# Performance work log

Hardware: AMD Instinct MI355X
Metric: run time of the kernel (lower is better)

Reference implementation:

```python
import jax, jax.numpy as jnp
import numpy as np

B, T, C, HEAD = 4, 4096, 1024, 64
SCALE = 1.0 / (C ** 0.5)  # module divides by embedding_size**0.5, not head_size**0.5


def setup_inputs() -> dict:
    key = jax.random.key(0)
    kx, kq, kk, kv = jax.random.split(key, 4)
    x = jax.random.normal(kx, (B, T, C), dtype=jnp.float32)
    # nn.Linear(C, head_size, bias=False) weights, stored as (C, head_size) for x @ W
    Wq = jax.random.normal(kq, (C, HEAD), dtype=jnp.float32) * (1.0 / np.sqrt(C))
    Wk = jax.random.normal(kk, (C, HEAD), dtype=jnp.float32) * (1.0 / np.sqrt(C))
    Wv = jax.random.normal(kv, (C, HEAD), dtype=jnp.float32) * (1.0 / np.sqrt(C))
    return {"x": x, "Wq": Wq, "Wk": Wk, "Wv": Wv}


def reference(x, Wq, Wk, Wv):
    q = jnp.einsum('btc,ch->bth', x, Wq)  # [B,T,HEAD]
    k = jnp.einsum('btc,ch->bth', x, Wk)
    v = jnp.einsum('btc,ch->bth', x, Wv)
    aff = jnp.einsum('bqh,bkh->bqk', q, k) * SCALE  # [B,T,T]
    causal = jnp.tril(jnp.ones((T, T), dtype=bool))
    aff = jnp.where(causal, aff, -jnp.inf)
    p = jax.nn.softmax(aff, axis=-1)  # dropout p=0.0 -> identity
    return jnp.einsum('bqk,bkh->bqh', p, v)  # [B,T,HEAD]
```

## Files before the change

### kernel.cpp

```cpp
#include <hip/hip_runtime.h>

#define T_SEQ 4096
#define NBATCH 4
#define CDIM 1024
#define NHEAD 64
#define SCALE (1.0f / 32.0f)
#define BT (NBATCH * T_SEQ)
#define NW 12
#define WREG 8960
#define PSTR 9

typedef __bf16 bf16x8 __attribute__((ext_vector_type(8)));
typedef float f32x4 __attribute__((ext_vector_type(4)));
typedef unsigned long long u64;

__device__ __forceinline__ unsigned short f2bf(float f) {
  union { float f; unsigned u; } x;
  x.f = f;
  unsigned r = x.u + 0x7FFFu + ((x.u >> 16) & 1u);
  return (unsigned short)(r >> 16);
}

__device__ __forceinline__ unsigned pack_bf16(float lo, float hi) {
  return (unsigned)f2bf(lo) | ((unsigned)f2bf(hi) << 16);
}

__device__ __forceinline__ f32x4 mfma16(bf16x8 a, bf16x8 b, f32x4 c) {
  return __builtin_amdgcn_mfma_f32_16x16x32_bf16(a, b, c, 0, 0, 0);
}

__device__ __forceinline__ bf16x8 ones8() {
  bf16x8 v;
  for (int j = 0; j < 8; ++j) v[j] = (__bf16)1.0f;
  return v;
}

__global__ void prep_w(const float* __restrict__ Wq, const float* __restrict__ Wk,
                       const float* __restrict__ Wv, unsigned short* __restrict__ Wt) {
  int c = blockIdx.x;
  const float* W = (c < 64) ? Wq : (c < 128) ? Wk : Wv;
  int cc = c & 63;
  float sc = (c < 64) ? SCALE : 1.0f;
  for (int k = threadIdx.x; k < CDIM; k += blockDim.x)
    Wt[c * CDIM + k] = f2bf(W[k * NHEAD + cc] * sc);
}

__global__ __launch_bounds__(256) void proj_qkv(
    const float* __restrict__ x, const unsigned short* __restrict__ Wt,
    unsigned short* __restrict__ qws, unsigned short* __restrict__ kws,
    unsigned short* __restrict__ vtws) {
  __shared__ unsigned short xlds[32][136];
  const int tid = threadIdx.x;
  const int lane = tid & 63;
  const int w = tid >> 6;
  const int g = lane >> 4;
  const int c15 = lane & 15;
  const int rb = blockIdx.x * 32;

  f32x4 acc[2][3];
  for (int i = 0; i < 2; i++)
    for (int j = 0; j < 3; j++) acc[i][j] = (f32x4){0.f, 0.f, 0.f, 0.f};

  const int sr = tid >> 3;
  const int scc = (tid & 7) * 16;
  const float* xrow = x + (size_t)(rb + sr) * CDIM + scc;

  float4 cur[4];
  for (int i = 0; i < 4; i++) cur[i] = *(const float4*)(xrow + i * 4);

  for (int k0 = 0; k0 < CDIM; k0 += 128) {
    unsigned short pk[16];
    for (int i = 0; i < 4; i++) {
      pk[i * 4 + 0] = f2bf(cur[i].x);
      pk[i * 4 + 1] = f2bf(cur[i].y);
      pk[i * 4 + 2] = f2bf(cur[i].z);
      pk[i * 4 + 3] = f2bf(cur[i].w);
    }
    *(bf16x8*)&xlds[sr][scc] = *(bf16x8*)&pk[0];
    *(bf16x8*)&xlds[sr][scc + 8] = *(bf16x8*)&pk[8];
    __syncthreads();
    if (k0 + 128 < CDIM)
      for (int i = 0; i < 4; i++)
        cur[i] = *(const float4*)(xrow + k0 + 128 + i * 4);

    for (int kk = 0; kk < 4; kk++) {
      bf16x8 a[2];
      for (int mt = 0; mt < 2; mt++)
        a[mt] = *(bf16x8*)&xlds[mt * 16 + c15][kk * 32 + g * 8];
      for (int bn = 0; bn < 3; bn++) {
        int col = w * 48 + bn * 16 + c15;
        bf16x8 bfrag =
            *(const bf16x8*)&Wt[(size_t)col * CDIM + k0 + kk * 32 + g * 8];
        for (int mt = 0; mt < 2; mt++)
          acc[mt][bn] = mfma16(a[mt], bfrag, acc[mt][bn]);
      }
    }
    __syncthreads();
  }

  for (int mt = 0; mt < 2; mt++)
    for (int bn = 0; bn < 3; bn++) {
      int col = w * 48 + bn * 16 + c15;
      int row0 = rb + mt * 16 + 4 * g;
      for (int r = 0; r < 4; r++) {
        unsigned short v = f2bf(acc[mt][bn][r]);
        int t = row0 + r;
        if (col < 64)
          qws[(size_t)t * 64 + col] = v;
        else if (col < 128)
          kws[(size_t)t * 64 + (col - 64)] = v;
        else
          vtws[(size_t)(col - 128) * BT + t] = v;
      }
    }
}

__global__ __launch_bounds__(768, 3) void attn_fwd(
    const unsigned short* __restrict__ qws, const unsigned short* __restrict__ kws,
    const unsigned short* __restrict__ vtws, float* __restrict__ out) {
  __shared__ __align__(16) char smem[NW * WREG];
  const int tid = threadIdx.x;
  const int lane = tid & 63;
  const int w = tid >> 6;
  const int g = lane >> 4;
  const int c = lane & 15;
  const int b = blockIdx.x >> 6;
  const int pi = blockIdx.x & 63;
  const size_t rowbase = (size_t)b * T_SEQ;
  char* wbase = smem + w * WREG;
  u64* pl = (u64*)wbase;
  const bf16x8 vone = ones8();

  for (int half = 0; half < 2; ++half) {
    const int qt = half ? (127 - pi) : pi;
    const int qb = qt * 32;
    const int nsteps = qt + 1;

    bf16x8 qf[2][2];
    for (int mi = 0; mi < 2; mi++)
      for (int hc = 0; hc < 2; hc++)
        qf[mi][hc] = *(const bf16x8*)&qws[(rowbase + qb + mi * 16 + c) * 64 +
                                          hc * 32 + g * 8];

    f32x4 o[2][4];
    f32x4 o5[2];
    float mrow[2];
    for (int mi = 0; mi < 2; mi++) {
      for (int nt = 0; nt < 4; nt++) o[mi][nt] = (f32x4){0.f, 0.f, 0.f, 0.f};
      o5[mi] = (f32x4){0.f, 0.f, 0.f, 0.f};
      mrow[mi] = -1e30f;
    }

    for (int st = w; st < nsteps; st += NW) {
      const int kt = st * 32;
      bf16x8 kc0[2], kc1[2], vc[4];
      for (int kn = 0; kn < 2; kn++) {
        kc0[kn] = *(const bf16x8*)&kws[(rowbase + kt + kn * 16 + c) * 64 + g * 8];
        kc1[kn] =
            *(const bf16x8*)&kws[(rowbase + kt + kn * 16 + c) * 64 + 32 + g * 8];
      }
      for (int nt = 0; nt < 4; nt++)
        vc[nt] =
            *(const bf16x8*)&vtws[(size_t)(nt * 16 + c) * BT + rowbase + kt + g * 8];

      f32x4 sv[2][2];
      for (int mi = 0; mi < 2; mi++)
        for (int kn = 0; kn < 2; kn++) {
          f32x4 z = (f32x4){0.f, 0.f, 0.f, 0.f};
          z = mfma16(kc0[kn], qf[mi][0], z);
          sv[mi][kn] = mfma16(kc1[kn], qf[mi][1], z);
        }

      if (st == nsteps - 1) {
        for (int mi = 0; mi < 2; mi++)
          for (int kn = 0; kn < 2; kn++)
            for (int r = 0; r < 4; r++) {
              int key = kt + kn * 16 + 4 * g + r;
              int qr = qb + mi * 16 + c;
              if (key > qr) sv[mi][kn][r] = -1e30f;
            }
      }

      for (int mi = 0; mi < 2; mi++) {
        float t = fmaxf(
            fmaxf(fmaxf(sv[mi][0][0], sv[mi][0][1]),
                  fmaxf(sv[mi][0][2], sv[mi][0][3])),
            fmaxf(fmaxf(sv[mi][1][0], sv[mi][1][1]),
                  fmaxf(sv[mi][1][2], sv[mi][1][3])));
        t = fmaxf(t, __shfl_xor(t, 16));
        t = fmaxf(t, __shfl_xor(t, 32));
        if (__any(t > mrow[mi] + 8.0f)) {
          float mn = fmaxf(mrow[mi], t);
          float a = __expf(mrow[mi] - mn);
          mrow[mi] = mn;
          for (int nt = 0; nt < 4; nt++) o[mi][nt] *= a;
          o5[mi] *= a;
        }
        for (int kn = 0; kn < 2; kn++)
          for (int r = 0; r < 4; r++)
            sv[mi][kn][r] = __expf(sv[mi][kn][r] - mrow[mi]);
        unsigned d0 = pack_bf16(sv[mi][0][0], sv[mi][0][1]);
        unsigned d1 = pack_bf16(sv[mi][0][2], sv[mi][0][3]);
        unsigned d2 = pack_bf16(sv[mi][1][0], sv[mi][1][1]);
        unsigned d3 = pack_bf16(sv[mi][1][2], sv[mi][1][3]);
        int row = mi * 16 + c;
        pl[row * PSTR + g] = ((u64)d1 << 32) | d0;
        pl[row * PSTR + 4 + g] = ((u64)d3 << 32) | d2;
      }

      asm volatile("" ::: "memory");

      for (int mi = 0; mi < 2; mi++) {
        union { u64 q[2]; bf16x8 v; } pu;
        pu.q[0] = pl[(mi * 16 + c) * PSTR + 2 * g];
        pu.q[1] = pl[(mi * 16 + c) * PSTR + 2 * g + 1];
        bf16x8 pa = pu.v;
        for (int nt = 0; nt < 4; nt++)
          o[mi][nt] = mfma16(vc[nt], pa, o[mi][nt]);
        o5[mi] = mfma16(vone, pa, o5[mi]);
      }
    }

    float* ow = (float*)wbase;
    float* mw = (float*)(wbase + 8704);
    float* lw = (float*)(wbase + 8832);
    for (int mi = 0; mi < 2; mi++)
      for (int nt = 0; nt < 4; nt++)
        for (int r = 0; r < 4; r++)
          ow[(mi * 16 + c) * 68 + nt * 16 + 4 * g + r] = o[mi][nt][r];
    if (g == 0)
      for (int mi = 0; mi < 2; mi++) {
        mw[mi * 16 + c] = mrow[mi];
        lw[mi * 16 + c] = o5[mi][0];
      }
    __syncthreads();

    for (int i = 0; i < 3; i++) {
      int e = tid + i * 768;
      if (e < 2048) {
        int row = e >> 6;
        int d = e & 63;
        float M = -1e30f;
        for (int ww = 0; ww < NW; ww++)
          M = fmaxf(M, ((const float*)(smem + ww * WREG + 8704))[row]);
        float L = 0.f, O = 0.f;
        for (int ww = 0; ww < NW; ww++) {
          float mv = ((const float*)(smem + ww * WREG + 8704))[row];
          float f = __expf(mv - M);
          L += f * ((const float*)(smem + ww * WREG + 8832))[row];
          O += f * ((const float*)(smem + ww * WREG))[row * 68 + d];
        }
        out[(rowbase + qb + row) * 64 + d] = O / L;
      }
    }
    __syncthreads();
  }
}

extern "C" void kernel_launch(void* const* d_in, const int* in_sizes, int n_in,
                              void* d_out, int out_size, void* d_ws, size_t ws_size,
                              hipStream_t stream) {
  const float* x = (const float*)d_in[0];
  const float* Wq = (const float*)d_in[1];
  const float* Wk = (const float*)d_in[2];
  const float* Wv = (const float*)d_in[3];
  float* out = (float*)d_out;

  char* ws = (char*)d_ws;
  unsigned short* Wt = (unsigned short*)(ws);
  unsigned short* qws = (unsigned short*)(ws + 393216);
  unsigned short* kws = (unsigned short*)(ws + 393216 + 2097152);
  unsigned short* vtws = (unsigned short*)(ws + 393216 + 2 * 2097152);

  prep_w<<<dim3(192), dim3(256), 0, stream>>>(Wq, Wk, Wv, Wt);
  proj_qkv<<<dim3(512), dim3(256), 0, stream>>>(x, Wt, qws, kws, vtws);
  attn_fwd<<<dim3(256), dim3(768), 0, stream>>>(qws, kws, vtws, out);
}
```

Before: 84.09 us.

## Split attention into one q-tile per block with register double-buffered K/V prefetch

The attention kernel now launches 512 blocks of 8 waves, each handling one 32-row query tile, instead of 256 blocks of 12 waves each looping over two tiles. It adds register double-buffering so the next K/V step's loads are issued before the current step's compute. Softmax moves to base-2 exponentials by folding log2(e) into the Q weight scale, and bf16 packing uses the hardware v_cvt_pk_bf16_f32 instruction. The aim is better load balance and latency hiding at the cost of more registers per wave. The lazy-rescale threshold also rises to 11 in log2 units, and cvt_pk's rounding may differ slightly from the manual round-to-nearest-even.

```diff
diff --git a/kernel.cpp b/kernel.cpp
--- a/kernel.cpp
+++ b/kernel.cpp
@@ -5,10 +5,12 @@
 #define CDIM 1024
 #define NHEAD 64
 #define SCALE (1.0f / 32.0f)
+#define LOG2E 1.4426950408889634f
 #define BT (NBATCH * T_SEQ)
-#define NW 12
+#define NW 8
 #define WREG 8960
 #define PSTR 9
+#define THR2 11.0f
 
 typedef __bf16 bf16x8 __attribute__((ext_vector_type(8)));
 typedef float f32x4 __attribute__((ext_vector_type(4)));
@@ -21,8 +23,10 @@
   return (unsigned short)(r >> 16);
 }
 
-__device__ __forceinline__ unsigned pack_bf16(float lo, float hi) {
-  return (unsigned)f2bf(lo) | ((unsigned)f2bf(hi) << 16);
+__device__ __forceinline__ unsigned cvt_pk(float lo, float hi) {
+  unsigned d;
+  asm("v_cvt_pk_bf16_f32 %0, %1, %2" : "=v"(d) : "v"(lo), "v"(hi));
+  return d;
 }
 
 __device__ __forceinline__ f32x4 mfma16(bf16x8 a, bf16x8 b, f32x4 c) {
@@ -40,7 +44,7 @@
   int c = blockIdx.x;
   const float* W = (c < 64) ? Wq : (c < 128) ? Wk : Wv;
   int cc = c & 63;
-  float sc = (c < 64) ? SCALE : 1.0f;
+  float sc = (c < 64) ? (SCALE * LOG2E) : 1.0f;
   for (int k = threadIdx.x; k < CDIM; k += blockDim.x)
     Wt[c * CDIM + k] = f2bf(W[k * NHEAD + cc] * sc);
 }
@@ -115,7 +119,7 @@
     }
 }
 
-__global__ __launch_bounds__(768, 3) void attn_fwd(
+__global__ __launch_bounds__(512, 4) void attn_fwd(
     const unsigned short* __restrict__ qws, const unsigned short* __restrict__ kws,
     const unsigned short* __restrict__ vtws, float* __restrict__ out) {
   __shared__ __align__(16) char smem[NW * WREG];
@@ -124,136 +128,146 @@
   const int w = tid >> 6;
   const int g = lane >> 4;
   const int c = lane & 15;
-  const int b = blockIdx.x >> 6;
-  const int pi = blockIdx.x & 63;
+  const int b = blockIdx.x >> 7;
+  const int j = blockIdx.x & 127;
+  const int qt = (j & 1) ? (127 - (j >> 1)) : (j >> 1);
+  const int qb = qt * 32;
+  const int nsteps = qt + 1;
   const size_t rowbase = (size_t)b * T_SEQ;
   char* wbase = smem + w * WREG;
   u64* pl = (u64*)wbase;
   const bf16x8 vone = ones8();
 
-  for (int half = 0; half < 2; ++half) {
-    const int qt = half ? (127 - pi) : pi;
-    const int qb = qt * 32;
-    const int nsteps = qt + 1;
-
-    bf16x8 qf[2][2];
+  bf16x8 qf[2][2];
+  for (int mi = 0; mi < 2; mi++)
+    for (int hc = 0; hc < 2; hc++)
+      qf[mi][hc] = *(const bf16x8*)&qws[(rowbase + qb + mi * 16 + c) * 64 +
+                                        hc * 32 + g * 8];
+
+  f32x4 o[2][4];
+  f32x4 o5[2];
+  float mrow[2];
+  for (int mi = 0; mi < 2; mi++) {
+    for (int nt = 0; nt < 4; nt++) o[mi][nt] = (f32x4){0.f, 0.f, 0.f, 0.f};
+    o5[mi] = (f32x4){0.f, 0.f, 0.f, 0.f};
+    mrow[mi] = -1e30f;
+  }
+
+  auto PREF = [&](int st, bf16x8 (&k0)[2], bf16x8 (&k1)[2], bf16x8 (&v)[4]) {
+    const int kt = st * 32;
+    for (int kn = 0; kn < 2; kn++) {
+      k0[kn] = *(const bf16x8*)&kws[(rowbase + kt + kn * 16 + c) * 64 + g * 8];
+      k1[kn] =
+          *(const bf16x8*)&kws[(rowbase + kt + kn * 16 + c) * 64 + 32 + g * 8];
+    }
+    for (int nt = 0; nt < 4; nt++)
+      v[nt] =
+          *(const bf16x8*)&vtws[(size_t)(nt * 16 + c) * BT + rowbase + kt + g * 8];
+  };
+
+  auto COMPUTE = [&](int st, bf16x8 (&k0)[2], bf16x8 (&k1)[2], bf16x8 (&v)[4]) {
+    const int kt = st * 32;
+    f32x4 sv[2][2];
     for (int mi = 0; mi < 2; mi++)
-      for (int hc = 0; hc < 2; hc++)
-        qf[mi][hc] = *(const bf16x8*)&qws[(rowbase + qb + mi * 16 + c) * 64 +
-                                          hc * 32 + g * 8];
-
-    f32x4 o[2][4];
-    f32x4 o5[2];
-    float mrow[2];
+      for (int kn = 0; kn < 2; kn++) {
+        f32x4 z = (f32x4){0.f, 0.f, 0.f, 0.f};
+        z = mfma16(k0[kn], qf[mi][0], z);
+        sv[mi][kn] = mfma16(k1[kn], qf[mi][1], z);
+      }
+
+    if (st == nsteps - 1) {
+      for (int mi = 0; mi < 2; mi++)
+        for (int kn = 0; kn < 2; kn++)
+          for (int r = 0; r < 4; r++) {
+            int key = kt + kn * 16 + 4 * g + r;
+            int qr = qb + mi * 16 + c;
+            if (key > qr) sv[mi][kn][r] = -1e30f;
+          }
+    }
+
     for (int mi = 0; mi < 2; mi++) {
-      for (int nt = 0; nt < 4; nt++) o[mi][nt] = (f32x4){0.f, 0.f, 0.f, 0.f};
-      o5[mi] = (f32x4){0.f, 0.f, 0.f, 0.f};
-      mrow[mi] = -1e30f;
-    }
-
-    for (int st = w; st < nsteps; st += NW) {
-      const int kt = st * 32;
-      bf16x8 kc0[2], kc1[2], vc[4];
-      for (int kn = 0; kn < 2; kn++) {
-        kc0[kn] = *(const bf16x8*)&kws[(rowbase + kt + kn * 16 + c) * 64 + g * 8];
-        kc1[kn] =
-            *(const bf16x8*)&kws[(rowbase + kt + kn * 16 + c) * 64 + 32 + g * 8];
-      }
+      float t = fmaxf(
+          fmaxf(fmaxf(sv[mi][0][0], sv[mi][0][1]),
+                fmaxf(sv[mi][0][2], sv[mi][0][3])),
+          fmaxf(fmaxf(sv[mi][1][0], sv[mi][1][1]),
+                fmaxf(sv[mi][1][2], sv[mi][1][3])));
+      t = fmaxf(t, __shfl_xor(t, 16));
+      t = fmaxf(t, __shfl_xor(t, 32));
+      if (__any(t > mrow[mi] + THR2)) {
+        float mn = fmaxf(mrow[mi], t);
+        float a = exp2f(mrow[mi] - mn);
+        mrow[mi] = mn;
+        for (int nt = 0; nt < 4; nt++) o[mi][nt] *= a;
+        o5[mi] *= a;
+      }
+      float p[8];
+      for (int kn = 0; kn < 2; kn++)
+        for (int r = 0; r < 4; r++)
+          p[kn * 4 + r] = exp2f(sv[mi][kn][r] - mrow[mi]);
+      unsigned d0 = cvt_pk(p[0], p[1]);
+      unsigned d1 = cvt_pk(p[2], p[3]);
+      unsigned d2 = cvt_pk(p[4], p[5]);
+      unsigned d3 = cvt_pk(p[6], p[7]);
+      int row = mi * 16 + c;
+      pl[row * PSTR + g] = ((u64)d1 << 32) | d0;
+      pl[row * PSTR + 4 + g] = ((u64)d3 << 32) | d2;
+    }
+
+    asm volatile("" ::: "memory");
+
+    for (int mi = 0; mi < 2; mi++) {
+      union { u64 q[2]; bf16x8 v8; } pu;
+      pu.q[0] = pl[(mi * 16 + c) * PSTR + 2 * g];
+      pu.q[1] = pl[(mi * 16 + c) * PSTR + 2 * g + 1];
+      bf16x8 pa = pu.v8;
       for (int nt = 0; nt < 4; nt++)
-        vc[nt] =
-            *(const bf16x8*)&vtws[(size_t)(nt * 16 + c) * BT + rowbase + kt + g * 8];
-
-      f32x4 sv[2][2];
-      for (int mi = 0; mi < 2; mi++)
-        for (int kn = 0; kn < 2; kn++) {
-          f32x4 z = (f32x4){0.f, 0.f, 0.f, 0.f};
-          z = mfma16(kc0[kn], qf[mi][0], z);
-          sv[mi][kn] = mfma16(kc1[kn], qf[mi][1], z);
-        }
-
-      if (st == nsteps - 1) {
-        for (int mi = 0; mi < 2; mi++)
-          for (int kn = 0; kn < 2; kn++)
-            for (int r = 0; r < 4; r++) {
-              int key = kt + kn * 16 + 4 * g + r;
-              int qr = qb + mi * 16 + c;
-              if (key > qr) sv[mi][kn][r] = -1e30f;
-            }
-      }
-
-      for (int mi = 0; mi < 2; mi++) {
-        float t = fmaxf(
-            fmaxf(fmaxf(sv[mi][0][0], sv[mi][0][1]),
-                  fmaxf(sv[mi][0][2], sv[mi][0][3])),
-            fmaxf(fmaxf(sv[mi][1][0], sv[mi][1][1]),
-                  fmaxf(sv[mi][1][2], sv[mi][1][3])));
-        t = fmaxf(t, __shfl_xor(t, 16));
-        t = fmaxf(t, __shfl_xor(t, 32));
-        if (__any(t > mrow[mi] + 8.0f)) {
-          float mn = fmaxf(mrow[mi], t);
-          float a = __expf(mrow[mi] - mn);
-          mrow[mi] = mn;
-          for (int nt = 0; nt < 4; nt++) o[mi][nt] *= a;
-          o5[mi] *= a;
-        }
-        for (int kn = 0; kn < 2; kn++)
-          for (int r = 0; r < 4; r++)
-            sv[mi][kn][r] = __expf(sv[mi][kn][r] - mrow[mi]);
-        unsigned d0 = pack_bf16(sv[mi][0][0], sv[mi][0][1]);
-        unsigned d1 = pack_bf16(sv[mi][0][2], sv[mi][0][3]);
-        unsigned d2 = pack_bf16(sv[mi][1][0], sv[mi][1][1]);
-        unsigned d3 = pack_bf16(sv[mi][1][2], sv[mi][1][3]);
-        int row = mi * 16 + c;
-        pl[row * PSTR + g] = ((u64)d1 << 32) | d0;
-        pl[row * PSTR + 4 + g] = ((u64)d3 << 32) | d2;
-      }
-
-      asm volatile("" ::: "memory");
-
-      for (int mi = 0; mi < 2; mi++) {
-        union { u64 q[2]; bf16x8 v; } pu;
-        pu.q[0] = pl[(mi * 16 + c) * PSTR + 2 * g];
-        pu.q[1] = pl[(mi * 16 + c) * PSTR + 2 * g + 1];
-        bf16x8 pa = pu.v;
-        for (int nt = 0; nt < 4; nt++)
-          o[mi][nt] = mfma16(vc[nt], pa, o[mi][nt]);
-        o5[mi] = mfma16(vone, pa, o5[mi]);
-      }
-    }
-
-    float* ow = (float*)wbase;
-    float* mw = (float*)(wbase + 8704);
-    float* lw = (float*)(wbase + 8832);
-    for (int mi = 0; mi < 2; mi++)
-      for (int nt = 0; nt < 4; nt++)
-        for (int r = 0; r < 4; r++)
-          ow[(mi * 16 + c) * 68 + nt * 16 + 4 * g + r] = o[mi][nt][r];
-    if (g == 0)
-      for (int mi = 0; mi < 2; mi++) {
-        mw[mi * 16 + c] = mrow[mi];
-        lw[mi * 16 + c] = o5[mi][0];
-      }
-    __syncthreads();
-
-    for (int i = 0; i < 3; i++) {
-      int e = tid + i * 768;
-      if (e < 2048) {
-        int row = e >> 6;
-        int d = e & 63;
-        float M = -1e30f;
-        for (int ww = 0; ww < NW; ww++)
-          M = fmaxf(M, ((const float*)(smem + ww * WREG + 8704))[row]);
-        float L = 0.f, O = 0.f;
-        for (int ww = 0; ww < NW; ww++) {
-          float mv = ((const float*)(smem + ww * WREG + 8704))[row];
-          float f = __expf(mv - M);
-          L += f * ((const float*)(smem + ww * WREG + 8832))[row];
-          O += f * ((const float*)(smem + ww * WREG))[row * 68 + d];
-        }
-        out[(rowbase + qb + row) * 64 + d] = O / L;
-      }
-    }
-    __syncthreads();
+        o[mi][nt] = mfma16(v[nt], pa, o[mi][nt]);
+      o5[mi] = mfma16(vone, pa, o5[mi]);
+    }
+  };
+
+  bf16x8 ka0[2], ka1[2], va[4], kb0[2], kb1[2], vb[4];
+  if (w < nsteps) PREF(w, ka0, ka1, va);
+  int st = w;
+  while (st < nsteps) {
+    if (st + NW < nsteps) PREF(st + NW, kb0, kb1, vb);
+    COMPUTE(st, ka0, ka1, va);
+    st += NW;
+    if (st >= nsteps) break;
+    if (st + NW < nsteps) PREF(st + NW, ka0, ka1, va);
+    COMPUTE(st, kb0, kb1, vb);
+    st += NW;
+  }
+
+  float* ow = (float*)wbase;
+  float* mw = (float*)(wbase + 8704);
+  float* lw = (float*)(wbase + 8832);
+  for (int mi = 0; mi < 2; mi++)
+    for (int nt = 0; nt < 4; nt++)
+      for (int r = 0; r < 4; r++)
+        ow[(mi * 16 + c) * 68 + nt * 16 + 4 * g + r] = o[mi][nt][r];
+  if (g == 0)
+    for (int mi = 0; mi < 2; mi++) {
+      mw[mi * 16 + c] = mrow[mi];
+      lw[mi * 16 + c] = o5[mi][0];
+    }
+  __syncthreads();
+
+  for (int i = 0; i < 4; i++) {
+    int e = tid + i * 512;
+    int row = e >> 6;
+    int d = e & 63;
+    float M = -1e30f;
+    for (int ww = 0; ww < NW; ww++)
+      M = fmaxf(M, ((const float*)(smem + ww * WREG + 8704))[row]);
+    float L = 0.f, O = 0.f;
+    for (int ww = 0; ww < NW; ww++) {
+      float mv = ((const float*)(smem + ww * WREG + 8704))[row];
+      float f = exp2f(mv - M);
+      L += f * ((const float*)(smem + ww * WREG + 8832))[row];
+      O += f * ((const float*)(smem + ww * WREG))[row * 68 + d];
+    }
+    out[(rowbase + qb + row) * 64 + d] = O / L;
   }
 }
 
@@ -274,5 +288,5 @@
 
   prep_w<<<dim3(192), dim3(256), 0, stream>>>(Wq, Wk, Wv, Wt);
   proj_qkv<<<dim3(512), dim3(256), 0, stream>>>(x, Wt, qws, kws, vtws);
-  attn_fwd<<<dim3(256), dim3(768), 0, stream>>>(qws, kws, vtws, out);
-}
+  attn_fwd<<<dim3(512), dim3(512), 0, stream>>>(qws, kws, vtws, out);
+}
```

After: 231.5 us. 175% more time.
